# Kernel tuning notes

Hardware: AMD Instinct MI355X
Metric: run time of the kernel (lower is better)

The kernel has to match this reference:

```python
import jax, jax.numpy as jnp
import numpy as np

EPS = 1e-6


def setup_inputs() -> dict:
    key = jax.random.key(0)
    T, B, D, n, K = 2048, 16, 1024, 64, 3
    k0, k1, k2 = jax.random.split(key, 3)
    x = jax.random.normal(k0, (T, B, D), dtype=jnp.float32)
    # xavier-ish scale for projections
    scale = 1.0 / np.sqrt(D).astype(np.float32)
    W_kv = jax.random.normal(k1, (K * 2 * n, D), dtype=jnp.float32) * scale
    W_q = jax.random.normal(k2, (n, D), dtype=jnp.float32) * scale
    B_gates = jnp.full((K, n), 2.0, dtype=jnp.float32)  # init.constant_(B_gates, 2.0)
    M_init = jnp.zeros((K, B, n, n), dtype=jnp.float32)
    return {"x": x, "M_init": M_init, "W_kv": W_kv, "W_q": W_q, "B_gates": B_gates}


def reference(x, M_init, W_kv, W_q, B_gates):
    # x: [T, B, D]; M_init: [K, B, n, n]; W_kv: [K*2*n, D]; W_q: [n, D]; B_gates: [K, n]
    T, B, D = x.shape
    K, n = B_gates.shape
    # fused kv projection, interleaved per level: [T, B, K, 2, n]
    kv = jnp.einsum('tbd,pd->tbp', x, W_kv).reshape(T, B, K, 2, n)
    k_all = jnp.transpose(kv[:, :, :, 0, :], (0, 2, 1, 3))  # [T, K, B, n]
    v_all = jnp.transpose(kv[:, :, :, 1, :], (0, 2, 1, 3))  # [T, K, B, n]
    q_all = jnp.einsum('tbd,nd->tbn', x, W_q)                # [T, B, n]
    b = B_gates[:, None, :]                                  # [K, 1, n] broadcast over batch

    def step(M, inputs):
        # M: [K, B, n, n]
        k_t, v_t, q_t = inputs
        k_norm = k_t / (jnp.linalg.norm(k_t, axis=-1, keepdims=True) + EPS)  # [K,B,n]
        gater = jnp.roll(M, shift=-1, axis=0)  # gater for level i is M[(i+1) % K]
        row_gate = jax.nn.sigmoid(jnp.einsum('kbij,kbj->kbi', gater, k_norm) + b)
        col_gate = jax.nn.sigmoid(jnp.einsum('kbji,kbj->kbi', gater, k_norm) + b)
        retrieved = jnp.einsum('kbij,kbj->kbi', M, k_norm)
        delta = v_t - retrieved
        M_new = (row_gate[..., None] * M * col_gate[:, :, None, :]
                 + jnp.einsum('kbi,kbj->kbij', delta, k_norm))
        Sq = jnp.einsum('bij,bj->bi', M_new[0], q_t)  # query against tower 0
        out = Sq * jax.nn.sigmoid(Sq)                  # self-gated output (SiLU self-gate)
        return M_new, out

    M_final, outputs = jax.lax.scan(step, M_init, (k_all, v_all, q_all))
    return outputs, M_final  # [T, B, n], [K, B, n, n]
```

## Files before the change

kernel.cpp:

```cpp
#include <hip/hip_runtime.h>
#include <hip/hip_bf16.h>
#include <math.h>

#define TT 2048
#define BB_ 16
#define DD 1024
#define NN 64
#define KK 3
#define PP 448

typedef float  v2f  __attribute__((ext_vector_type(2)));
typedef float  f4   __attribute__((ext_vector_type(4)));
typedef float  f32x4 __attribute__((ext_vector_type(4)));
typedef short  bh8  __attribute__((ext_vector_type(8)));

__device__ __forceinline__ float sigmoidf_(float x) {
    return 1.0f / (1.0f + __expf(-x));
}

#define LDS_BARRIER() __asm__ volatile("s_waitcnt lgkmcnt(0)\n\ts_barrier" ::: "memory")

template<int CTRL>
__device__ __forceinline__ float dpp_mov(float v) {
    int r = __builtin_amdgcn_update_dpp(0, __float_as_int(v), CTRL, 0xF, 0xF, true);
    return __int_as_float(r);
}

__device__ __forceinline__ float sel16_dpp(const float v[4], int s) {
    const int s0 = s & 1, s1 = (s >> 1) & 1;
    float k0 = s0 ? v[1] : v[0], d0 = s0 ? v[0] : v[1];
    float k1 = s0 ? v[3] : v[2], d1 = s0 ? v[2] : v[3];
    float a0 = k0 + dpp_mov<0xB1>(d0);
    float a1 = k1 + dpp_mov<0xB1>(d1);
    float kb = s1 ? a1 : a0, db = s1 ? a0 : a1;
    float r  = kb + dpp_mov<0x4E>(db);
    r += dpp_mov<0x124>(r);
    r += dpp_mov<0x128>(r);
    return r;
}

__global__ __launch_bounds__(256) void cvt_w_kernel(
    const float* __restrict__ Wkv,
    const float* __restrict__ Wq,
    unsigned short* __restrict__ Wsw)
{
    const int n = blockIdx.x;
    const int tid = threadIdx.x;
    const float* row = (n < 384) ? (Wkv + (size_t)n * DD)
                                 : (Wq  + (size_t)(n - 384) * DD);
    const int idx = tid * 4;
    const int kb = idx >> 5, kk = idx & 31;
    float4 f = *(const float4*)(row + idx);
    __hip_bfloat162 h0 = __float22bfloat162_rn(make_float2(f.x, f.y));
    __hip_bfloat162 h1 = __float22bfloat162_rn(make_float2(f.z, f.w));
    unsigned u0, u1;
    __builtin_memcpy(&u0, &h0, 4);
    __builtin_memcpy(&u1, &h1, 4);
    ushort4 o = make_ushort4((unsigned short)u0, (unsigned short)(u0 >> 16),
                             (unsigned short)u1, (unsigned short)(u1 >> 16));
    *(ushort4*)&Wsw[((size_t)kb * PP + n) * 32 + kk] = o;
}

__global__ __launch_bounds__(256) void mfma_proj_kernel(
    const float* __restrict__ x,
    const unsigned short* __restrict__ Wsw,
    float* __restrict__ kvq)
{
    const int tid  = threadIdx.x;
    const int w    = tid >> 6;
    const int lane = tid & 63;
    const int ln   = lane & 15;
    const int quad = lane >> 4;
    const int m0   = blockIdx.x * 64;

    f32x4 acc[28];
    #pragma unroll
    for (int t = 0; t < 28; ++t) acc[t] = (f32x4){0.f, 0.f, 0.f, 0.f};

    const float* xrow = x + (size_t)(m0 + 16 * w + ln) * DD + quad * 8;

    for (int kb = 0; kb < 32; ++kb) {
        float4 a0 = *(const float4*)(xrow + kb * 32);
        float4 a1 = *(const float4*)(xrow + kb * 32 + 4);
        __hip_bfloat162 h0 = __float22bfloat162_rn(make_float2(a0.x, a0.y));
        __hip_bfloat162 h1 = __float22bfloat162_rn(make_float2(a0.z, a0.w));
        __hip_bfloat162 h2 = __float22bfloat162_rn(make_float2(a1.x, a1.y));
        __hip_bfloat162 h3 = __float22bfloat162_rn(make_float2(a1.z, a1.w));
        unsigned u0, u1, u2, u3;
        __builtin_memcpy(&u0, &h0, 4); __builtin_memcpy(&u1, &h1, 4);
        __builtin_memcpy(&u2, &h2, 4); __builtin_memcpy(&u3, &h3, 4);
        bh8 a;
        a[0] = (short)u0; a[1] = (short)(u0 >> 16);
        a[2] = (short)u1; a[3] = (short)(u1 >> 16);
        a[4] = (short)u2; a[5] = (short)(u2 >> 16);
        a[6] = (short)u3; a[7] = (short)(u3 >> 16);

        const unsigned short* wp_ = Wsw + (size_t)kb * PP * 32 + quad * 8;
        #pragma unroll
        for (int t = 0; t < 28; ++t) {
            const bh8 bfr = *(const bh8*)(wp_ + (16 * t + ln) * 32);
            acc[t] = __builtin_amdgcn_mfma_f32_16x16x32_bf16(a, bfr, acc[t], 0, 0, 0);
        }
    }

    #pragma unroll
    for (int g = 0; g < 3; ++g) {
        const int t0 = g * 8;
        #pragma unroll
        for (int reg = 0; reg < 4; ++reg) {
            float ss = acc[t0][reg] * acc[t0][reg]
                     + acc[t0 + 1][reg] * acc[t0 + 1][reg]
                     + acc[t0 + 2][reg] * acc[t0 + 2][reg]
                     + acc[t0 + 3][reg] * acc[t0 + 3][reg];
            #pragma unroll
            for (int m = 1; m <= 8; m <<= 1) ss += __shfl_xor(ss, m, 64);
            const float sc = 1.0f / (sqrtf(ss) + 1e-6f);
            #pragma unroll
            for (int t = t0; t < t0 + 4; ++t) acc[t][reg] *= sc;
        }
    }

    float* orow = kvq + (size_t)(m0 + 16 * w + quad * 4) * PP + ln;
    #pragma unroll
    for (int t = 0; t < 28; ++t)
        #pragma unroll
        for (int reg = 0; reg < 4; ++reg)
            orow[(size_t)reg * PP + 16 * t] = acc[t][reg];
}

__global__ __launch_bounds__(768) void scan_kernel(
    const float* __restrict__ kvq,
    const float* __restrict__ M_init,
    const float* __restrict__ B_gates,
    float* __restrict__ d_out)
{
    const int b    = blockIdx.x;
    const int tid  = threadIdx.x;
    const int wid  = tid >> 6;
    const int k    = wid >> 2;
    const int q    = wid & 3;
    const int lane = tid & 63;
    const int tr   = lane >> 4;
    const int tc   = lane & 15;
    const int kp   = (k + 2) % 3;
    const int row0 = 16 * q + 4 * tr;
    const int col0 = 4 * tc;
    const int s3   = tc & 3;
    const int rowS = row0 + s3;

    __shared__ __align__(16) float rg_lds[2][3][64];
    __shared__ __align__(16) float cs_part[2][3][4][4][64];
    __shared__ __align__(16) float cg_lds[2][3][64];
    __shared__ __align__(16) float dl_lds[2][3][64];

    v2f M2[4][2];
    #pragma unroll
    for (int i = 0; i < 4; ++i) {
        f4 t = *(const f4*)(M_init + (((size_t)k * BB_ + b) * NN + row0 + i) * NN + col0);
        M2[i][0] = (v2f){t.x, t.y};
        M2[i][1] = (v2f){t.z, t.w};
    }

    const float bias_pub_r = B_gates[kp * NN + rowS];
    const int  isComb = (wid >= 4) && (wid < 7);
    const int  cls    = isComb ? (wid - 4) : 0;
    const float cbias = isComb ? B_gates[cls * NN + lane] : 0.f;

    float* outp = d_out;
    float* Mout = d_out + (size_t)TT * BB_ * NN;

    const int o_knc = k * 128 + col0;
    const int o_wpc = kp * 128 + col0;
    const int o_wpr = kp * 128 + row0;
    const int o_v   = k * 128 + 64 + rowS;
    const int o_q   = 384 + col0;

    const float* kvt = kvq + (size_t)b * PP;

    f4 sK[2], sC[2], sR[2], sQ[2];
    float sV[2];
    sK[0] = *(const f4*)(kvt + o_knc);
    sC[0] = *(const f4*)(kvt + o_wpc);
    sR[0] = *(const f4*)(kvt + o_wpr);
    sV[0] = kvt[o_v];
    sQ[0] = (f4){0.f, 0.f, 0.f, 0.f};
    if (k == 0) sQ[0] = *(const f4*)(kvt + o_q);
    f4 qp = sQ[0];

    #pragma unroll 2
    for (int t = 0; t < TT; ++t) {
        const int pb  = t & 1;
        const int cur = t & 1, nxt = cur ^ 1;

        const float* kvn = (t + 1 < TT) ? (kvt + (size_t)BB_ * PP) : kvt;
        sK[nxt] = *(const f4*)(kvn + o_knc);
        sC[nxt] = *(const f4*)(kvn + o_wpc);
        sR[nxt] = *(const f4*)(kvn + o_wpr);
        sV[nxt] = kvn[o_v];
        if (k == 0) sQ[nxt] = *(const f4*)(kvn + o_q);

        const v2f kn2a = {sK[cur].x, sK[cur].y}, kn2b = {sK[cur].z, sK[cur].w};
        const v2f wc2a = {sC[cur].x, sC[cur].y}, wc2b = {sC[cur].z, sC[cur].w};

        v2f cp2a, cp2b;
        {
            const v2f w0 = {sR[cur].x, sR[cur].x};
            cp2a = M2[0][0] * w0;
            cp2b = M2[0][1] * w0;
        }
        #pragma unroll
        for (int i = 1; i < 4; ++i) {
            const float w = (i == 1) ? sR[cur].y : (i == 2) ? sR[cur].z : sR[cur].w;
            const v2f wv = {w, w};
            cp2a += M2[i][0] * wv;
            cp2b += M2[i][1] * wv;
        }
        *(f4*)&cs_part[pb][kp][q][tr][col0] = (f4){cp2a.x, cp2a.y, cp2b.x, cp2b.y};

        v2f rp2[4], sp2[4];
        #pragma unroll
        for (int i = 0; i < 4; ++i) {
            rp2[i] = M2[i][0] * kn2a + M2[i][1] * kn2b;
            sp2[i] = M2[i][0] * wc2a + M2[i][1] * wc2b;
        }
        float rp[4], sp[4];
        #pragma unroll
        for (int i = 0; i < 4; ++i) { rp[i] = rp2[i].x + rp2[i].y; sp[i] = sp2[i].x + sp2[i].y; }

        const float rsv = sel16_dpp(sp, s3);
        const float rtv = sel16_dpp(rp, s3);
        const float dv  = sV[cur] - rtv;

        if (tc < 4) {
            rg_lds[pb][kp][rowS] = sigmoidf_(rsv + bias_pub_r);
            dl_lds[pb][k][rowS]  = dv;
        }
        LDS_BARRIER();

        const f4 rg4 = *(const f4*)&rg_lds[pb][k][row0];
        const f4 dl4 = *(const f4*)&dl_lds[pb][k][row0];
        if (isComb) {
            float s0 = cs_part[pb][cls][0][0][lane] + cs_part[pb][cls][0][1][lane]
                     + cs_part[pb][cls][0][2][lane] + cs_part[pb][cls][0][3][lane];
            float s1 = cs_part[pb][cls][1][0][lane] + cs_part[pb][cls][1][1][lane]
                     + cs_part[pb][cls][1][2][lane] + cs_part[pb][cls][1][3][lane];
            float s2 = cs_part[pb][cls][2][0][lane] + cs_part[pb][cls][2][1][lane]
                     + cs_part[pb][cls][2][2][lane] + cs_part[pb][cls][2][3][lane];
            float s3_ = cs_part[pb][cls][3][0][lane] + cs_part[pb][cls][3][1][lane]
                     + cs_part[pb][cls][3][2][lane] + cs_part[pb][cls][3][3][lane];
            cg_lds[pb][cls][lane] = sigmoidf_((s0 + s1) + (s2 + s3_) + cbias);
        }
        if (k == 0) {
            const v2f qpa = {qp.x, qp.y}, qpb = {qp.z, qp.w};
            float op[4];
            #pragma unroll
            for (int i = 0; i < 4; ++i) {
                v2f o2 = M2[i][0] * qpa + M2[i][1] * qpb;
                op[i] = o2.x + o2.y;
            }
            const float ov = sel16_dpp(op, s3);
            if (t > 0 && tc < 4)
                outp[((size_t)(t - 1) * BB_ + b) * NN + rowS] = ov * sigmoidf_(ov);
        }
        LDS_BARRIER();

        const f4 cg4 = *(const f4*)&cg_lds[pb][k][col0];
        const v2f cg2a = {cg4.x, cg4.y}, cg2b = {cg4.z, cg4.w};
        #pragma unroll
        for (int i = 0; i < 4; ++i) {
            const float rgi = (i == 0) ? rg4.x : (i == 1) ? rg4.y : (i == 2) ? rg4.z : rg4.w;
            const float ddi = (i == 0) ? dl4.x : (i == 1) ? dl4.y : (i == 2) ? dl4.z : dl4.w;
            const v2f r2 = {rgi, rgi};
            const v2f d2 = {ddi, ddi};
            M2[i][0] = r2 * (M2[i][0] * cg2a) + d2 * kn2a;
            M2[i][1] = r2 * (M2[i][1] * cg2b) + d2 * kn2b;
        }

        qp  = sQ[cur];
        kvt = kvn;
    }

    if (k == 0) {
        const v2f qpa = {qp.x, qp.y}, qpb = {qp.z, qp.w};
        float op[4];
        #pragma unroll
        for (int i = 0; i < 4; ++i) {
            v2f o2 = M2[i][0] * qpa + M2[i][1] * qpb;
            op[i] = o2.x + o2.y;
        }
        const float ov = sel16_dpp(op, s3);
        if (tc < 4)
            outp[((size_t)(TT - 1) * BB_ + b) * NN + rowS] = ov * sigmoidf_(ov);
    }

    #pragma unroll
    for (int i = 0; i < 4; ++i) {
        f4 v = (f4){M2[i][0].x, M2[i][0].y, M2[i][1].x, M2[i][1].y};
        *(f4*)&Mout[(((size_t)k * BB_ + b) * NN + row0 + i) * NN + col0] = v;
    }
}

extern "C" void kernel_launch(void* const* d_in, const int* in_sizes, int n_in,
                              void* d_out, int out_size, void* d_ws, size_t ws_size,
                              hipStream_t stream) {
    const float* x       = (const float*)d_in[0];
    const float* M_init  = (const float*)d_in[1];
    const float* W_kv    = (const float*)d_in[2];
    const float* W_q     = (const float*)d_in[3];
    const float* B_gates = (const float*)d_in[4];
    float* out = (float*)d_out;

    float* kvq = (float*)d_ws;
    const size_t kvq_bytes = (size_t)TT * BB_ * PP * 4;
    unsigned short* Wsw = (unsigned short*)((char*)d_ws + kvq_bytes);

    cvt_w_kernel<<<PP, 256, 0, stream>>>(W_kv, W_q, Wsw);
    mfma_proj_kernel<<<TT * BB_ / 64, 256, 0, stream>>>(x, Wsw, kvq);
    scan_kernel<<<BB_, 768, 0, stream>>>(kvq, M_init, B_gates, out);
}
```

Before: 2.237 ms.

## Reorder per-step barriers so column-gate reduction overlaps row-dot computation

Moves the first barrier to right after the column partial-sum stores. The combiner waves load their partials early and reduce them while the row and retrieval dot products run, and the row gate, delta and column gate all become visible at a single second barrier. The column-gate reduction is spread over six waves (two per level, each handling half the columns, with a cross-half shuffle) instead of three. Double-buffered LDS is dropped to single buffers, which relies on the barrier ordering to avoid cross-step races.

```diff
diff --git a/kernel.cpp b/kernel.cpp
--- a/kernel.cpp
+++ b/kernel.cpp
@@ -148,10 +148,10 @@
     const int s3   = tc & 3;
     const int rowS = row0 + s3;
 
-    __shared__ __align__(16) float rg_lds[2][3][64];
-    __shared__ __align__(16) float cs_part[2][3][4][4][64];
-    __shared__ __align__(16) float cg_lds[2][3][64];
-    __shared__ __align__(16) float dl_lds[2][3][64];
+    __shared__ __align__(16) float cs_lds[3][4][4][64];
+    __shared__ __align__(16) float rg_lds[3][64];
+    __shared__ __align__(16) float dl_lds[3][64];
+    __shared__ __align__(16) float cg_lds[3][64];
 
     v2f M2[4][2];
     #pragma unroll
@@ -162,9 +162,13 @@
     }
 
     const float bias_pub_r = B_gates[kp * NN + rowS];
-    const int  isComb = (wid >= 4) && (wid < 7);
-    const int  cls    = isComb ? (wid - 4) : 0;
-    const float cbias = isComb ? B_gates[cls * NN + lane] : 0.f;
+
+    const int  isComb = (wid >= 4) && (wid <= 9);
+    const int  cls    = isComb ? ((wid - 4) >> 1) : 0;
+    const int  hw     = (wid - 4) & 1;
+    const int  colC   = hw * 32 + (lane & 31);
+    const int  qsel   = lane >> 5;
+    const float cbias = isComb ? B_gates[cls * NN + colC] : 0.f;
 
     float* outp = d_out;
     float* Mout = d_out + (size_t)TT * BB_ * NN;
@@ -189,7 +193,6 @@
 
     #pragma unroll 2
     for (int t = 0; t < TT; ++t) {
-        const int pb  = t & 1;
         const int cur = t & 1, nxt = cur ^ 1;
 
         const float* kvn = (t + 1 < TT) ? (kvt + (size_t)BB_ * PP) : kvt;
@@ -199,9 +202,6 @@
         sV[nxt] = kvn[o_v];
         if (k == 0) sQ[nxt] = *(const f4*)(kvn + o_q);
 
-        const v2f kn2a = {sK[cur].x, sK[cur].y}, kn2b = {sK[cur].z, sK[cur].w};
-        const v2f wc2a = {sC[cur].x, sC[cur].y}, wc2b = {sC[cur].z, sC[cur].w};
-
         v2f cp2a, cp2b;
         {
             const v2f w0 = {sR[cur].x, sR[cur].x};
@@ -215,7 +215,20 @@
             cp2a += M2[i][0] * wv;
             cp2b += M2[i][1] * wv;
         }
-        *(f4*)&cs_part[pb][kp][q][tr][col0] = (f4){cp2a.x, cp2a.y, cp2b.x, cp2b.y};
+        *(f4*)&cs_lds[kp][q][tr][col0] = (f4){cp2a.x, cp2a.y, cp2b.x, cp2b.y};
+        LDS_BARRIER();
+
+        float cv[8];
+        if (isComb) {
+            #pragma unroll
+            for (int qq = 0; qq < 2; ++qq)
+                #pragma unroll
+                for (int tt = 0; tt < 4; ++tt)
+                    cv[qq * 4 + tt] = cs_lds[cls][2 * qsel + qq][tt][colC];
+        }
+
+        const v2f kn2a = {sK[cur].x, sK[cur].y}, kn2b = {sK[cur].z, sK[cur].w};
+        const v2f wc2a = {sC[cur].x, sC[cur].y}, wc2b = {sC[cur].z, sC[cur].w};
 
         v2f rp2[4], sp2[4];
         #pragma unroll
@@ -232,24 +245,18 @@
         const float dv  = sV[cur] - rtv;
 
         if (tc < 4) {
-            rg_lds[pb][kp][rowS] = sigmoidf_(rsv + bias_pub_r);
-            dl_lds[pb][k][rowS]  = dv;
-        }
-        LDS_BARRIER();
-
-        const f4 rg4 = *(const f4*)&rg_lds[pb][k][row0];
-        const f4 dl4 = *(const f4*)&dl_lds[pb][k][row0];
+            rg_lds[kp][rowS] = sigmoidf_(rsv + bias_pub_r);
+            dl_lds[k][rowS]  = dv;
+        }
+
         if (isComb) {
-            float s0 = cs_part[pb][cls][0][0][lane] + cs_part[pb][cls][0][1][lane]
-                     + cs_part[pb][cls][0][2][lane] + cs_part[pb][cls][0][3][lane];
-            float s1 = cs_part[pb][cls][1][0][lane] + cs_part[pb][cls][1][1][lane]
-                     + cs_part[pb][cls][1][2][lane] + cs_part[pb][cls][1][3][lane];
-            float s2 = cs_part[pb][cls][2][0][lane] + cs_part[pb][cls][2][1][lane]
-                     + cs_part[pb][cls][2][2][lane] + cs_part[pb][cls][2][3][lane];
-            float s3_ = cs_part[pb][cls][3][0][lane] + cs_part[pb][cls][3][1][lane]
-                     + cs_part[pb][cls][3][2][lane] + cs_part[pb][cls][3][3][lane];
-            cg_lds[pb][cls][lane] = sigmoidf_((s0 + s1) + (s2 + s3_) + cbias);
-        }
+            float s = ((cv[0] + cv[1]) + (cv[2] + cv[3]))
+                    + ((cv[4] + cv[5]) + (cv[6] + cv[7]));
+            s += __shfl_xor(s, 32, 64);
+            const float g = sigmoidf_(s + cbias);
+            if (lane < 32) cg_lds[cls][colC] = g;
+        }
+
         if (k == 0) {
             const v2f qpa = {qp.x, qp.y}, qpb = {qp.z, qp.w};
             float op[4];
@@ -264,7 +271,9 @@
         }
         LDS_BARRIER();
 
-        const f4 cg4 = *(const f4*)&cg_lds[pb][k][col0];
+        const f4 rg4 = *(const f4*)&rg_lds[k][row0];
+        const f4 dl4 = *(const f4*)&dl_lds[k][row0];
+        const f4 cg4 = *(const f4*)&cg_lds[k][col0];
         const v2f cg2a = {cg4.x, cg4.y}, cg2b = {cg4.z, cg4.w};
         #pragma unroll
         for (int i = 0; i < 4; ++i) {
```

New measurement: 2.614 ms. 16.9% more time.

## Offload column-gate reduction to dedicated warps in scan kernel

Applied to the files above, without the earlier changes.

Grows the scan block from 12 to 16 waves. The four extra waves only reduce the column-gate partial sums and apply the sigmoid, which moves that serial LDS reduction off the critical path of the matrix-owning waves. The barrier placement changes so the cs partials are published before the row and retrieval dot products, which lets the gate reduction overlap with them. In exchange the block is larger, and the barrier counts across the two wave groups must stay matched or the kernel deadlocks.

```diff
diff --git a/kernel.cpp b/kernel.cpp
--- a/kernel.cpp
+++ b/kernel.cpp
@@ -128,7 +128,7 @@
             orow[(size_t)reg * PP + 16 * t] = acc[t][reg];
 }
 
-__global__ __launch_bounds__(768) void scan_kernel(
+__global__ __launch_bounds__(1024) void scan_kernel(
     const float* __restrict__ kvq,
     const float* __restrict__ M_init,
     const float* __restrict__ B_gates,
@@ -137,9 +137,39 @@
     const int b    = blockIdx.x;
     const int tid  = threadIdx.x;
     const int wid  = tid >> 6;
+    const int lane = tid & 63;
+
+    __shared__ __align__(16) float cs_lds[2][3][4][4][64];
+    __shared__ __align__(16) float rg_lds[2][3][64];
+    __shared__ __align__(16) float dl_lds[2][3][64];
+    __shared__ __align__(16) float cg_lds[2][3][64];
+
+    if (wid >= 12) {
+        const int  act = (wid < 15);
+        const int  cls = act ? (wid - 12) : 0;
+        const float cbias = act ? B_gates[cls * NN + lane] : 0.f;
+        #pragma unroll 2
+        for (int t = 0; t < TT; ++t) {
+            const int pb = t & 1;
+            LDS_BARRIER();
+            if (act) {
+                float s0 = (cs_lds[pb][cls][0][0][lane] + cs_lds[pb][cls][0][1][lane])
+                         + (cs_lds[pb][cls][0][2][lane] + cs_lds[pb][cls][0][3][lane]);
+                float s1 = (cs_lds[pb][cls][1][0][lane] + cs_lds[pb][cls][1][1][lane])
+                         + (cs_lds[pb][cls][1][2][lane] + cs_lds[pb][cls][1][3][lane]);
+                float s2 = (cs_lds[pb][cls][2][0][lane] + cs_lds[pb][cls][2][1][lane])
+                         + (cs_lds[pb][cls][2][2][lane] + cs_lds[pb][cls][2][3][lane]);
+                float s3 = (cs_lds[pb][cls][3][0][lane] + cs_lds[pb][cls][3][1][lane])
+                         + (cs_lds[pb][cls][3][2][lane] + cs_lds[pb][cls][3][3][lane]);
+                cg_lds[pb][cls][lane] = sigmoidf_((s0 + s1) + (s2 + s3) + cbias);
+            }
+            LDS_BARRIER();
+        }
+        return;
+    }
+
     const int k    = wid >> 2;
     const int q    = wid & 3;
-    const int lane = tid & 63;
     const int tr   = lane >> 4;
     const int tc   = lane & 15;
     const int kp   = (k + 2) % 3;
@@ -148,11 +178,6 @@
     const int s3   = tc & 3;
     const int rowS = row0 + s3;
 
-    __shared__ __align__(16) float rg_lds[2][3][64];
-    __shared__ __align__(16) float cs_part[2][3][4][4][64];
-    __shared__ __align__(16) float cg_lds[2][3][64];
-    __shared__ __align__(16) float dl_lds[2][3][64];
-
     v2f M2[4][2];
     #pragma unroll
     for (int i = 0; i < 4; ++i) {
@@ -162,9 +187,6 @@
     }
 
     const float bias_pub_r = B_gates[kp * NN + rowS];
-    const int  isComb = (wid >= 4) && (wid < 7);
-    const int  cls    = isComb ? (wid - 4) : 0;
-    const float cbias = isComb ? B_gates[cls * NN + lane] : 0.f;
 
     float* outp = d_out;
     float* Mout = d_out + (size_t)TT * BB_ * NN;
@@ -199,9 +221,6 @@
         sV[nxt] = kvn[o_v];
         if (k == 0) sQ[nxt] = *(const f4*)(kvn + o_q);
 
-        const v2f kn2a = {sK[cur].x, sK[cur].y}, kn2b = {sK[cur].z, sK[cur].w};
-        const v2f wc2a = {sC[cur].x, sC[cur].y}, wc2b = {sC[cur].z, sC[cur].w};
-
         v2f cp2a, cp2b;
         {
             const v2f w0 = {sR[cur].x, sR[cur].x};
@@ -215,7 +234,11 @@
             cp2a += M2[i][0] * wv;
             cp2b += M2[i][1] * wv;
         }
-        *(f4*)&cs_part[pb][kp][q][tr][col0] = (f4){cp2a.x, cp2a.y, cp2b.x, cp2b.y};
+        *(f4*)&cs_lds[pb][kp][q][tr][col0] = (f4){cp2a.x, cp2a.y, cp2b.x, cp2b.y};
+        LDS_BARRIER();
+
+        const v2f kn2a = {sK[cur].x, sK[cur].y}, kn2b = {sK[cur].z, sK[cur].w};
+        const v2f wc2a = {sC[cur].x, sC[cur].y}, wc2b = {sC[cur].z, sC[cur].w};
 
         v2f rp2[4], sp2[4];
         #pragma unroll
@@ -239,17 +262,8 @@
 
         const f4 rg4 = *(const f4*)&rg_lds[pb][k][row0];
         const f4 dl4 = *(const f4*)&dl_lds[pb][k][row0];
-        if (isComb) {
-            float s0 = cs_part[pb][cls][0][0][lane] + cs_part[pb][cls][0][1][lane]
-                     + cs_part[pb][cls][0][2][lane] + cs_part[pb][cls][0][3][lane];
-            float s1 = cs_part[pb][cls][1][0][lane] + cs_part[pb][cls][1][1][lane]
-                     + cs_part[pb][cls][1][2][lane] + cs_part[pb][cls][1][3][lane];
-            float s2 = cs_part[pb][cls][2][0][lane] + cs_part[pb][cls][2][1][lane]
-                     + cs_part[pb][cls][2][2][lane] + cs_part[pb][cls][2][3][lane];
-            float s3_ = cs_part[pb][cls][3][0][lane] + cs_part[pb][cls][3][1][lane]
-                     + cs_part[pb][cls][3][2][lane] + cs_part[pb][cls][3][3][lane];
-            cg_lds[pb][cls][lane] = sigmoidf_((s0 + s1) + (s2 + s3_) + cbias);
-        }
+        const f4 cg4 = *(const f4*)&cg_lds[pb][k][col0];
+
         if (k == 0) {
             const v2f qpa = {qp.x, qp.y}, qpb = {qp.z, qp.w};
             float op[4];
@@ -262,9 +276,7 @@
             if (t > 0 && tc < 4)
                 outp[((size_t)(t - 1) * BB_ + b) * NN + rowS] = ov * sigmoidf_(ov);
         }
-        LDS_BARRIER();
-
-        const f4 cg4 = *(const f4*)&cg_lds[pb][k][col0];
+
         const v2f cg2a = {cg4.x, cg4.y}, cg2b = {cg4.z, cg4.w};
         #pragma unroll
         for (int i = 0; i < 4; ++i) {
@@ -316,5 +328,5 @@
 
     cvt_w_kernel<<<PP, 256, 0, stream>>>(W_kv, W_q, Wsw);
     mfma_proj_kernel<<<TT * BB_ / 64, 256, 0, stream>>>(x, Wsw, kvq);
-    scan_kernel<<<BB_, 768, 0, stream>>>(kvq, M_init, B_gates, out);
-}
+    scan_kernel<<<BB_, 1024, 0, stream>>>(kvq, M_init, B_gates, out);
+}
```

Result: faster. 2.079 ms (-7.0%).
